# Optimization experiments

Hardware: AMD Instinct MI355X
Metric: run time of the kernel (lower is better)

## Reference

```python
import jax, jax.numpy as jnp
import numpy as np

TEMPERATURE = 0.5
SCALE_LOSS = 1.0 / 32.0
LAMBDA = 0.0039


def setup_inputs() -> dict:
    key = jax.random.key(0)
    z = jax.random.normal(key, (4096, 6, 256), dtype=jnp.float32)
    return {"z": z}


def reference(z):
    B, V = z.shape[0], z.shape[1]
    # [B, V, ...] -> [V, B, D], L2-normalize embeddings
    zv = z.reshape(B, V, -1).transpose(1, 0, 2)
    zn = zv / jnp.linalg.norm(zv, axis=-1, keepdims=True)

    # Positive error: per-sample cross-view similarity [B, V, V]
    sim_pos = jnp.einsum('vbd,wbd->bvw', zn, zn)
    pos = jnp.exp((1.0 - sim_pos) / TEMPERATURE).mean(axis=(1, 2))  # [B]

    # Negative error: per-view within-batch similarity [V, B, B]
    sim_neg = jnp.exp(jnp.einsum('vbd,vcd->vbc', zn, zn) / TEMPERATURE)
    offdiag_mask = ~jnp.eye(B, dtype=bool)  # [B, B]
    off_mean = jnp.where(offdiag_mask[None], sim_neg, 0.0).sum(-1) / (B - 1)  # [V, B]
    neg = off_mean.sum(0)  # [B], accumulated over views

    return jnp.sum(pos) * SCALE_LOSS + LAMBDA * jnp.sum(neg)
```

## Files before the change

### kernel.cpp

```cpp
#include <hip/hip_runtime.h>
#include <cstdint>
#include <cstddef>

#define B_N 4096
#define V_N 6
#define D_N 256
#define NTILE 528
#define NBLK (NTILE * V_N)

typedef int i32x4 __attribute__((ext_vector_type(4)));

#define QC 298.0f
#define INV_C2_X2 (2.0f / (QC * QC))

__device__ __forceinline__ void async_load16(void* lds, const void* gmem) {
  __builtin_amdgcn_global_load_lds(
      (const __attribute__((address_space(1))) unsigned int*)gmem,
      (__attribute__((address_space(3))) unsigned int*)lds,
      16, 0, 0);
}

__global__ __launch_bounds__(256) void norm_pos_kernel(
    const float* __restrict__ z, signed char* __restrict__ znb,
    float* __restrict__ pos_part) {
  const int lane = threadIdx.x & 63;
  const int w = threadIdx.x >> 6;
  const int b = blockIdx.x * 4 + w;

  const float4* zb4 = (const float4*)(z + (size_t)b * (V_N * D_N));
  float4 x[V_N];
#pragma unroll
  for (int v = 0; v < V_N; ++v) x[v] = zb4[v * 64 + lane];

  float s[21];
  {
    int p = 0;
#pragma unroll
    for (int v = 0; v < V_N; ++v)
#pragma unroll
      for (int u = v; u < V_N; ++u) {
        s[p] = x[v].x * x[u].x + x[v].y * x[u].y +
               x[v].z * x[u].z + x[v].w * x[u].w;
        ++p;
      }
  }
#pragma unroll
  for (int off = 1; off < 64; off <<= 1)
#pragma unroll
    for (int q = 0; q < 21; ++q)
      s[q] += __shfl_xor(s[q], off);

  const int selfidx[V_N] = {0, 6, 11, 15, 18, 20};
  float inv[V_N];
#pragma unroll
  for (int v = 0; v < V_N; ++v) inv[v] = rsqrtf(s[selfidx[v]]);

#pragma unroll
  for (int v = 0; v < V_N; ++v) {
    const float sc = inv[v] * QC;
    int q0 = (int)rintf(fminf(127.0f, fmaxf(-127.0f, x[v].x * sc)));
    int q1 = (int)rintf(fminf(127.0f, fmaxf(-127.0f, x[v].y * sc)));
    int q2 = (int)rintf(fminf(127.0f, fmaxf(-127.0f, x[v].z * sc)));
    int q3 = (int)rintf(fminf(127.0f, fmaxf(-127.0f, x[v].w * sc)));
    int packed = (q0 & 255) | ((q1 & 255) << 8) | ((q2 & 255) << 16)
               | ((q3 & 255) << 24);
    ((int*)(znb + ((size_t)v * B_N + b) * D_N))[lane] = packed;
  }

  float psum = 0.0f;
  {
    int p = 0;
#pragma unroll
    for (int v = 0; v < V_N; ++v)
#pragma unroll
      for (int u = v; u < V_N; ++u) {
        if (u > v) psum += __expf(2.0f * (1.0f - s[p] * inv[v] * inv[u]));
        ++p;
      }
  }
  if (lane == 0) pos_part[b] = psum;
}

__global__ __launch_bounds__(256) void gram_kernel(
    const signed char* __restrict__ znb, float* __restrict__ neg_part) {
  const int v = blockIdx.y;
  const int t = blockIdx.x;
  int i = (int)((sqrtf(8.0f * (float)t + 1.0f) - 1.0f) * 0.5f);
  while ((i + 1) * (i + 2) / 2 <= t) ++i;
  while (i * (i + 1) / 2 > t) --i;
  const int j = t - i * (i + 1) / 2;

  const signed char* Zv = znb + (size_t)v * B_N * D_N;
  const signed char* Ag = Zv + (size_t)(i * 128) * D_N;
  const signed char* Bg = Zv + (size_t)(j * 128) * D_N;

  __shared__ signed char As[128][128];
  __shared__ signed char Bs[128][128];
  __shared__ float blk[4];

  const int tid = threadIdx.x;
  const int lane = tid & 63;
  const int w = tid >> 6;
  const int wr = w >> 1;
  const int wc = w & 1;

  i32x4 c[4][4];
#pragma unroll
  for (int a = 0; a < 4; ++a)
#pragma unroll
    for (int b2 = 0; b2 < 4; ++b2) c[a][b2] = (i32x4){0, 0, 0, 0};

  const int kc = lane >> 4;
  const int mrow = wr * 64 + (lane & 15);
  const int ncol = wc * 64 + (lane & 15);

  signed char* AsF = &As[0][0];
  signed char* BsF = &Bs[0][0];

  for (int k0 = 0; k0 < D_N; k0 += 128) {
    __syncthreads();
#pragma unroll
    for (int q = 0; q < 4; ++q) {
      const int s = tid + 256 * q;
      const int row = s >> 3;
      const int gc = (s & 7) ^ (row & 7);
      async_load16(AsF + s * 16, Ag + (size_t)row * D_N + k0 + gc * 16);
      async_load16(BsF + s * 16, Bg + (size_t)row * D_N + k0 + gc * 16);
    }
    __syncthreads();

#pragma unroll
    for (int kk = 0; kk < 2; ++kk) {
      const int cbase = kk * 4 + kc;
      i32x4 af[4], bfr[4];
#pragma unroll
      for (int f = 0; f < 4; ++f) {
        const int ra = mrow + 16 * f;
        const int rb2 = ncol + 16 * f;
        af[f]  = *(const i32x4*)(AsF + ra * 128 + ((cbase ^ (ra & 7)) * 16));
        bfr[f] = *(const i32x4*)(BsF + rb2 * 128 + ((cbase ^ (rb2 & 7)) * 16));
      }
#pragma unroll
      for (int fm = 0; fm < 4; ++fm)
#pragma unroll
        for (int fn = 0; fn < 4; ++fn)
          c[fm][fn] = __builtin_amdgcn_mfma_i32_16x16x64_i8(
              af[fm], bfr[fn], c[fm][fn], 0, 0, 0);
    }
  }

  float lsum = 0.0f;
  const int rb = i * 128 + wr * 64 + (lane >> 4) * 4;
  const int cb = j * 128 + wc * 64 + (lane & 15);
#pragma unroll
  for (int fm = 0; fm < 4; ++fm) {
#pragma unroll
    for (int fn = 0; fn < 4; ++fn) {
      const int gcol = cb + fn * 16;
#pragma unroll
      for (int r = 0; r < 4; ++r) {
        const int grow = rb + fm * 16 + r;
        float e = __expf((float)c[fm][fn][r] * INV_C2_X2);
        lsum += (grow == gcol) ? 0.0f : e;
      }
    }
  }
  if (i != j) lsum *= 2.0f;

#pragma unroll
  for (int off = 32; off > 0; off >>= 1) lsum += __shfl_down(lsum, off);
  if (lane == 0) blk[w] = lsum;
  __syncthreads();
  if (tid == 0) neg_part[t + NTILE * v] = blk[0] + blk[1] + blk[2] + blk[3];
}

__global__ __launch_bounds__(1024) void finalize_kernel(
    const float* __restrict__ pos_part, const float* __restrict__ neg_part,
    float* __restrict__ out) {
  const int t = threadIdx.x;
  const int lane = t & 63;
  const int w = t >> 6;
  __shared__ float pr[16], nr[16];

  float p = 0.0f;
  for (int idx = t; idx < B_N; idx += 1024) p += pos_part[idx];
  float n = 0.0f;
  for (int idx = t; idx < NBLK; idx += 1024) n += neg_part[idx];
#pragma unroll
  for (int off = 32; off > 0; off >>= 1) {
    p += __shfl_down(p, off);
    n += __shfl_down(n, off);
  }
  if (lane == 0) { pr[w] = p; nr[w] = n; }
  __syncthreads();
  if (t == 0) {
    float P = 0.0f, N = 0.0f;
#pragma unroll
    for (int k = 0; k < 16; ++k) { P += pr[k]; N += nr[k]; }
    out[0] = (1.0f / 32.0f) * ((float)B_N / 6.0f + P / 18.0f) +
             0.0039f * (N / (float)(B_N - 1));
  }
}

extern "C" void kernel_launch(void* const* d_in, const int* in_sizes, int n_in,
                              void* d_out, int out_size, void* d_ws, size_t ws_size,
                              hipStream_t stream) {
  const float* z = (const float*)d_in[0];
  float* out = (float*)d_out;
  float* pos_part = (float*)d_ws;
  float* neg_part = (float*)((char*)d_ws + 16384);
  signed char* znb = (signed char*)((char*)d_ws + 32768);

  norm_pos_kernel<<<B_N / 4, 256, 0, stream>>>(z, znb, pos_part);
  dim3 grid(NTILE, V_N, 1);
  gram_kernel<<<grid, 256, 0, stream>>>(znb, neg_part);
  finalize_kernel<<<1, 1024, 0, stream>>>(pos_part, neg_part, out);
}
```

Measured before the change: 100.4 us.

## Process four Gram tiles per block with double-buffered async LDS prefetch

```diff
diff --git a/kernel.cpp b/kernel.cpp
--- a/kernel.cpp
+++ b/kernel.cpp
@@ -7,6 +7,7 @@
 #define D_N 256
 #define NTILE 528
 #define NBLK (NTILE * V_N)
+#define TPB 4
 
 typedef int i32x4 __attribute__((ext_vector_type(4)));
 
@@ -84,18 +85,23 @@
 __global__ __launch_bounds__(256) void gram_kernel(
     const signed char* __restrict__ znb, float* __restrict__ neg_part) {
   const int v = blockIdx.y;
-  const int t = blockIdx.x;
-  int i = (int)((sqrtf(8.0f * (float)t + 1.0f) - 1.0f) * 0.5f);
-  while ((i + 1) * (i + 2) / 2 <= t) ++i;
-  while (i * (i + 1) / 2 > t) --i;
-  const int j = t - i * (i + 1) / 2;
+  const int tbase = blockIdx.x * TPB;
+
+  int ti[TPB], tj[TPB];
+#pragma unroll
+  for (int q = 0; q < TPB; ++q) {
+    const int t = tbase + q;
+    int i = (int)((sqrtf(8.0f * (float)t + 1.0f) - 1.0f) * 0.5f);
+    while ((i + 1) * (i + 2) / 2 <= t) ++i;
+    while (i * (i + 1) / 2 > t) --i;
+    ti[q] = i;
+    tj[q] = t - i * (i + 1) / 2;
+  }
 
   const signed char* Zv = znb + (size_t)v * B_N * D_N;
-  const signed char* Ag = Zv + (size_t)(i * 128) * D_N;
-  const signed char* Bg = Zv + (size_t)(j * 128) * D_N;
-
-  __shared__ signed char As[128][128];
-  __shared__ signed char Bs[128][128];
+
+  __shared__ signed char As[2][128][128];
+  __shared__ signed char Bs[2][128][128];
   __shared__ float blk[4];
 
   const int tid = threadIdx.x;
@@ -104,31 +110,41 @@
   const int wr = w >> 1;
   const int wc = w & 1;
 
-  i32x4 c[4][4];
-#pragma unroll
-  for (int a = 0; a < 4; ++a)
-#pragma unroll
-    for (int b2 = 0; b2 < 4; ++b2) c[a][b2] = (i32x4){0, 0, 0, 0};
-
   const int kc = lane >> 4;
   const int mrow = wr * 64 + (lane & 15);
   const int ncol = wc * 64 + (lane & 15);
 
-  signed char* AsF = &As[0][0];
-  signed char* BsF = &Bs[0][0];
-
-  for (int k0 = 0; k0 < D_N; k0 += 128) {
-    __syncthreads();
+  auto stage = [&](int c) {
+    const int tile = c >> 1;
+    const int ks = (c & 1) * 128;
+    const signed char* Ag = Zv + (size_t)(ti[tile] * 128) * D_N + ks;
+    const signed char* Bg = Zv + (size_t)(tj[tile] * 128) * D_N + ks;
+    signed char* Ad = &As[c & 1][0][0];
+    signed char* Bd = &Bs[c & 1][0][0];
 #pragma unroll
     for (int q = 0; q < 4; ++q) {
       const int s = tid + 256 * q;
       const int row = s >> 3;
       const int gc = (s & 7) ^ (row & 7);
-      async_load16(AsF + s * 16, Ag + (size_t)row * D_N + k0 + gc * 16);
-      async_load16(BsF + s * 16, Bg + (size_t)row * D_N + k0 + gc * 16);
+      async_load16(Ad + s * 16, Ag + (size_t)row * D_N + gc * 16);
+      async_load16(Bd + s * 16, Bg + (size_t)row * D_N + gc * 16);
     }
-    __syncthreads();
-
+  };
+
+  i32x4 c[4][4];
+#pragma unroll
+  for (int a = 0; a < 4; ++a)
+#pragma unroll
+    for (int b2 = 0; b2 < 4; ++b2) c[a][b2] = (i32x4){0, 0, 0, 0};
+
+  stage(0);
+  __syncthreads();
+
+  for (int ch = 0; ch < 2 * TPB; ++ch) {
+    if (ch + 1 < 2 * TPB) stage(ch + 1);
+
+    const signed char* AsF = &As[ch & 1][0][0];
+    const signed char* BsF = &Bs[ch & 1][0][0];
 #pragma unroll
     for (int kk = 0; kk < 2; ++kk) {
       const int cbase = kk * 4 + kc;
@@ -147,31 +163,39 @@
           c[fm][fn] = __builtin_amdgcn_mfma_i32_16x16x64_i8(
               af[fm], bfr[fn], c[fm][fn], 0, 0, 0);
     }
-  }
-
-  float lsum = 0.0f;
-  const int rb = i * 128 + wr * 64 + (lane >> 4) * 4;
-  const int cb = j * 128 + wc * 64 + (lane & 15);
-#pragma unroll
-  for (int fm = 0; fm < 4; ++fm) {
-#pragma unroll
-    for (int fn = 0; fn < 4; ++fn) {
-      const int gcol = cb + fn * 16;
-#pragma unroll
-      for (int r = 0; r < 4; ++r) {
-        const int grow = rb + fm * 16 + r;
-        float e = __expf((float)c[fm][fn][r] * INV_C2_X2);
-        lsum += (grow == gcol) ? 0.0f : e;
-      }
+
+    if (ch & 1) {
+      const int tile = ch >> 1;
+      const int i = ti[tile], j = tj[tile];
+      float lsum = 0.0f;
+      const int rb = i * 128 + wr * 64 + (lane >> 4) * 4;
+      const int cb = j * 128 + wc * 64 + (lane & 15);
+#pragma unroll
+      for (int fm = 0; fm < 4; ++fm) {
+#pragma unroll
+        for (int fn = 0; fn < 4; ++fn) {
+          const int gcol = cb + fn * 16;
+#pragma unroll
+          for (int r = 0; r < 4; ++r) {
+            const int grow = rb + fm * 16 + r;
+            float e = __expf((float)c[fm][fn][r] * INV_C2_X2);
+            lsum += (grow == gcol) ? 0.0f : e;
+          }
+          c[fm][fn] = (i32x4){0, 0, 0, 0};
+        }
+      }
+      if (i != j) lsum *= 2.0f;
+#pragma unroll
+      for (int off = 32; off > 0; off >>= 1) lsum += __shfl_down(lsum, off);
+      if (lane == 0) blk[w] = lsum;
     }
-  }
-  if (i != j) lsum *= 2.0f;
-
-#pragma unroll
-  for (int off = 32; off > 0; off >>= 1) lsum += __shfl_down(lsum, off);
-  if (lane == 0) blk[w] = lsum;
-  __syncthreads();
-  if (tid == 0) neg_part[t + NTILE * v] = blk[0] + blk[1] + blk[2] + blk[3];
+
+    __syncthreads();
+
+    if ((ch & 1) && tid == 0)
+      neg_part[tbase + (ch >> 1) + NTILE * v] =
+          blk[0] + blk[1] + blk[2] + blk[3];
+  }
 }
 
 __global__ __launch_bounds__(1024) void finalize_kernel(
@@ -212,7 +236,7 @@
   signed char* znb = (signed char*)((char*)d_ws + 32768);
 
   norm_pos_kernel<<<B_N / 4, 256, 0, stream>>>(z, znb, pos_part);
-  dim3 grid(NTILE, V_N, 1);
+  dim3 grid(NTILE / TPB, V_N, 1);
   gram_kernel<<<grid, 256, 0, stream>>>(znb, neg_part);
   finalize_kernel<<<1, 1024, 0, stream>>>(pos_part, neg_part, out);
 }
```

Result: slower. 110.2 us (+9.8%).
